# Performance work log

Measured on AMD Instinct MI355X. Metric: run time of the kernel, lower is better.

The kernel has to match this reference:

```python
import jax, jax.numpy as jnp
import numpy as np

TTT_LR = 0.01
LN_EPS = 1e-5


def setup_inputs() -> dict:
    key = jax.random.key(0)
    ks = jax.random.split(key, 4)
    B, S, D, DS = 4, 2048, 1024, 64
    sc = 1.0 / np.sqrt(D).astype(np.float32)
    return {
        "x": jax.random.normal(ks[0], (B, S, D), dtype=jnp.float32),
        "Wk": jax.random.normal(ks[1], (DS, D), dtype=jnp.float32) * sc,
        "bk": jnp.zeros((DS,), jnp.float32),
        "Wv": jax.random.normal(ks[2], (D, D), dtype=jnp.float32) * sc,
        "bv": jnp.zeros((D,), jnp.float32),
        "Wq": jax.random.normal(ks[3], (DS, D), dtype=jnp.float32) * sc,
        "bq": jnp.zeros((DS,), jnp.float32),
        "gamma": jnp.ones((D,), jnp.float32),
        "beta": jnp.zeros((D,), jnp.float32),
    }


def reference(x, Wk, bk, Wv, bv, Wq, bq, gamma, beta):
    B, S, D = x.shape
    DS = Wk.shape[0]
    # LayerNorm over last dim
    mu = jnp.mean(x, axis=-1, keepdims=True)
    var = jnp.mean((x - mu) ** 2, axis=-1, keepdims=True)
    h = (x - mu) * jax.lax.rsqrt(var + LN_EPS) * gamma + beta
    # projections: keys/queries (B,S,DS), values (B,S,D)
    keys = jnp.einsum('bsd,ed->bse', h, Wk) + bk
    values = jnp.einsum('bsd,ed->bse', h, Wv) + bv
    queries = jnp.einsum('bsd,ed->bse', h, Wq) + bq

    def step(W, qkv):
        # W: (B, D, DS) fast-weight state
        q_t, k_t, v_t = qkv  # (B,DS), (B,DS), (B,D)
        y_t = jnp.einsum('bds,bs->bd', W, q_t)      # read with query
        pred = jnp.einsum('bds,bs->bd', W, k_t)     # predict with key
        err = pred - v_t                             # (B, D)
        W = W - TTT_LR * err[:, :, None] * k_t[:, None, :]  # rank-1 grad step
        return W, y_t

    W0 = jnp.zeros((B, D, DS), x.dtype)
    # scan over time: inputs as (S, B, ...)
    qs = jnp.swapaxes(queries, 0, 1)
    ks_ = jnp.swapaxes(keys, 0, 1)
    vs = jnp.swapaxes(values, 0, 1)
    _, ys = jax.lax.scan(step, W0, (qs, ks_, vs))   # ys: (S, B, D)
    y = jnp.swapaxes(ys, 0, 1)
    return x + y
```

## Files before the change

### kernel.cpp

```cpp
#include <hip/hip_runtime.h>
#include <hip/hip_bf16.h>

#define TTT_LR 0.01f
#define LN_EPS 1e-5f

#define BB 4
#define SS 2048
#define DD 1024
#define DSZ 64
#define CHUNK 64
#define NC (SS / CHUNK)
#define NCAT 1152
#define MiB (1024ull * 1024ull)

typedef __hip_bfloat16 bf16;
typedef __bf16 bf16x8 __attribute__((ext_vector_type(8)));
typedef float f32x4 __attribute__((ext_vector_type(4)));

__device__ __forceinline__ void gload_lds16(const void* g, void* l) {
    __builtin_amdgcn_global_load_lds(
        (const __attribute__((address_space(1))) unsigned int*)g,
        (__attribute__((address_space(3))) unsigned int*)l, 16, 0, 0);
}

__global__ __launch_bounds__(256) void cvt_cat_kernel(
    const float* __restrict__ Wk, const float* __restrict__ Wq,
    const float* __restrict__ Wv, bf16* __restrict__ Wcat)
{
    const int i = blockIdx.x * 256 + threadIdx.x;
    if (i >= NCAT * DD / 4) return;
    const int idx = i * 4;
    const int row = idx >> 10, col = idx & 1023;
    const float* src = (row < 64)  ? (Wk + (size_t)row * DD)
                     : (row < 128) ? (Wq + (size_t)(row - 64) * DD)
                                   : (Wv + (size_t)(row - 128) * DD);
    float4 v = *reinterpret_cast<const float4*>(src + col);
    bf16 h4[4] = {__float2bfloat16(v.x), __float2bfloat16(v.y),
                  __float2bfloat16(v.z), __float2bfloat16(v.w)};
    *reinterpret_cast<ushort4*>(Wcat + idx) = *reinterpret_cast<ushort4*>(h4);
}

__global__ __launch_bounds__(256) void ln_kernel(
    const float* __restrict__ x, const float* __restrict__ gamma,
    const float* __restrict__ beta, bf16* __restrict__ hb)
{
    __shared__ float wsum[4], wsum2[4];
    const int row = blockIdx.x, tid = threadIdx.x;
    const int lane = tid & 63, wave = tid >> 6;

    float4 v0 = *reinterpret_cast<const float4*>(x + (size_t)row * DD + tid * 4);
    float s = v0.x + v0.y + v0.z + v0.w;
    float s2 = fmaf(v0.x, v0.x, fmaf(v0.y, v0.y, fmaf(v0.z, v0.z, v0.w * v0.w)));
    #pragma unroll
    for (int off = 32; off > 0; off >>= 1) {
        s  += __shfl_down(s, off, 64);
        s2 += __shfl_down(s2, off, 64);
    }
    if (lane == 0) { wsum[wave] = s; wsum2[wave] = s2; }
    __syncthreads();
    s  = wsum[0] + wsum[1] + wsum[2] + wsum[3];
    s2 = wsum2[0] + wsum2[1] + wsum2[2] + wsum2[3];
    const float mu = s * (1.0f / DD);
    const float rs = rsqrtf(s2 * (1.0f / DD) - mu * mu + LN_EPS);

    float4 g  = *reinterpret_cast<const float4*>(gamma + tid * 4);
    float4 be = *reinterpret_cast<const float4*>(beta + tid * 4);
    bf16 h4[4];
    h4[0] = __float2bfloat16((v0.x - mu) * rs * g.x + be.x);
    h4[1] = __float2bfloat16((v0.y - mu) * rs * g.y + be.y);
    h4[2] = __float2bfloat16((v0.z - mu) * rs * g.z + be.z);
    h4[3] = __float2bfloat16((v0.w - mu) * rs * g.w + be.w);
    *reinterpret_cast<ushort4*>(hb + (size_t)row * DD + tid * 4) =
        *reinterpret_cast<ushort4*>(h4);
}

__global__ __launch_bounds__(256) void kqv_kernel(
    const bf16* __restrict__ h, const bf16* __restrict__ Wcat,
    const float* __restrict__ bk, const float* __restrict__ bq,
    const float* __restrict__ bv,
    float* __restrict__ kbuf, float* __restrict__ qbuf, bf16* __restrict__ vbuf16)
{
    __shared__ bf16 Ash[128 * 64];
    __shared__ bf16 Bsh[128 * 64];
    const int tid = threadIdx.x, lane = tid & 63, wave = tid >> 6;
    const int m = lane & 15, quad = lane >> 4;
    const int wr = wave >> 1, wc = wave & 1;
    const int m0 = blockIdx.y * 128;
    const int n0 = blockIdx.x * 128;

    const int srow = wave * 8 + (lane >> 3);
    const int scb = lane & 7;

    f32x4 acc[4][4] = {};

    for (int k0 = 0; k0 < DD; k0 += 64) {
        __syncthreads();
        #pragma unroll
        for (int i = 0; i < 4; ++i) {
            const int row = i * 32 + srow;
            const int g16 = scb ^ (row & 7);
            gload_lds16(h    + (size_t)(m0 + row) * DD + k0 + g16 * 8,
                        (char*)Ash + (size_t)(i * 32 + wave * 8) * 128);
            gload_lds16(Wcat + (size_t)(n0 + row) * DD + k0 + g16 * 8,
                        (char*)Bsh + (size_t)(i * 32 + wave * 8) * 128);
        }
        __syncthreads();
        #pragma unroll
        for (int ks = 0; ks < 2; ++ks) {
            bf16x8 af[4], bfr[4];
            #pragma unroll
            for (int mt = 0; mt < 4; ++mt) {
                const int row = wr * 64 + mt * 16 + m;
                const int kb = (ks * 4 + quad) ^ (row & 7);
                af[mt] = *reinterpret_cast<const bf16x8*>(&Ash[row * 64 + kb * 8]);
            }
            #pragma unroll
            for (int nt = 0; nt < 4; ++nt) {
                const int row = wc * 64 + nt * 16 + m;
                const int kb = (ks * 4 + quad) ^ (row & 7);
                bfr[nt] = *reinterpret_cast<const bf16x8*>(&Bsh[row * 64 + kb * 8]);
            }
            #pragma unroll
            for (int mt = 0; mt < 4; ++mt)
                #pragma unroll
                for (int nt = 0; nt < 4; ++nt)
                    acc[mt][nt] = __builtin_amdgcn_mfma_f32_16x16x32_bf16(
                        af[mt], bfr[nt], acc[mt][nt], 0, 0, 0);
        }
    }

    #pragma unroll
    for (int nt = 0; nt < 4; ++nt) {
        const int n = n0 + wc * 64 + nt * 16 + m;
        if (n < 64) {
            const float bias = bk[n];
            #pragma unroll
            for (int mt = 0; mt < 4; ++mt) {
                const int row = m0 + wr * 64 + mt * 16 + quad * 4;
                #pragma unroll
                for (int r = 0; r < 4; ++r)
                    kbuf[(size_t)(row + r) * DSZ + n] = acc[mt][nt][r] + bias;
            }
        } else if (n < 128) {
            const float bias = bq[n - 64];
            #pragma unroll
            for (int mt = 0; mt < 4; ++mt) {
                const int row = m0 + wr * 64 + mt * 16 + quad * 4;
                #pragma unroll
                for (int r = 0; r < 4; ++r)
                    qbuf[(size_t)(row + r) * DSZ + (n - 64)] = acc[mt][nt][r] + bias;
            }
        } else {
            const float bias = bv[n - 128];
            #pragma unroll
            for (int mt = 0; mt < 4; ++mt) {
                const int row = m0 + wr * 64 + mt * 16 + quad * 4;
                #pragma unroll
                for (int r = 0; r < 4; ++r)
                    vbuf16[(size_t)(row + r) * DD + (n - 128)] =
                        __float2bfloat16(acc[mt][nt][r] + bias);
            }
        }
    }
}

__global__ __launch_bounds__(256) void prep_kernel(
    const float* __restrict__ kbuf, const float* __restrict__ qbuf,
    bf16* __restrict__ Mb16, bf16* __restrict__ AMb16,
    bf16* __restrict__ Bb16, bf16* __restrict__ Qtb16, bf16* __restrict__ Ktb16)
{
    __shared__ bf16 K16[64 * 72];
    __shared__ bf16 Kt16[64 * 72];
    __shared__ bf16 Q16[64 * 72];
    __shared__ bf16 Astl[64 * 72];
    __shared__ bf16 Minv16[64 * 72];
    __shared__ bf16 MinvT16[64 * 72];
    __shared__ bf16 BnegT[64 * 72];
    __shared__ float Gf[64 * 65];
    __shared__ float Mf[64 * 65];

    const int c = blockIdx.x, b = blockIdx.y;
    const int tid = threadIdx.x, lane = tid & 63, w = tid >> 6;
    const int m = lane & 15, quad = lane >> 4;
    const float* kp = kbuf + ((size_t)b * SS + c * 64) * DSZ;
    const float* qp = qbuf + ((size_t)b * SS + c * 64) * DSZ;
    const size_t cb = ((size_t)b * NC + c) * 4096;

    #pragma unroll
    for (int it = 0; it < 4; ++it) {
        const int f4 = tid + it * 256;
        const int t = f4 >> 4;
        const int s = (f4 & 15) * 4;
        float4 kv = *reinterpret_cast<const float4*>(kp + t * DSZ + s);
        float4 qv = *reinterpret_cast<const float4*>(qp + t * DSZ + s);
        bf16 kb4[4] = {__float2bfloat16(kv.x), __float2bfloat16(kv.y),
                       __float2bfloat16(kv.z), __float2bfloat16(kv.w)};
        bf16 qb4[4] = {__float2bfloat16(qv.x), __float2bfloat16(qv.y),
                       __float2bfloat16(qv.z), __float2bfloat16(qv.w)};
        *reinterpret_cast<ushort4*>(&K16[t * 72 + s]) = *reinterpret_cast<ushort4*>(kb4);
        *reinterpret_cast<ushort4*>(&Q16[t * 72 + s]) = *reinterpret_cast<ushort4*>(qb4);
        #pragma unroll
        for (int i = 0; i < 4; ++i) Kt16[(s + i) * 72 + t] = kb4[i];
    }
    __syncthreads();

    bf16x8 afK[2], afQ[2], bfK[4][2];
    #pragma unroll
    for (int ks = 0; ks < 2; ++ks) {
        afK[ks] = *reinterpret_cast<const bf16x8*>(&K16[(w * 16 + m) * 72 + ks * 32 + quad * 8]);
        afQ[ks] = *reinterpret_cast<const bf16x8*>(&Q16[(w * 16 + m) * 72 + ks * 32 + quad * 8]);
        #pragma unroll
        for (int nt = 0; nt < 4; ++nt)
            bfK[nt][ks] = *reinterpret_cast<const bf16x8*>(&K16[(nt * 16 + m) * 72 + ks * 32 + quad * 8]);
    }
    f32x4 gacc[4] = {}, aacc[4] = {};
    #pragma unroll
    for (int ks = 0; ks < 2; ++ks)
        #pragma unroll
        for (int nt = 0; nt < 4; ++nt) {
            gacc[nt] = __builtin_amdgcn_mfma_f32_16x16x32_bf16(afK[ks], bfK[nt][ks], gacc[nt], 0, 0, 0);
            aacc[nt] = __builtin_amdgcn_mfma_f32_16x16x32_bf16(afQ[ks], bfK[nt][ks], aacc[nt], 0, 0, 0);
        }
    #pragma unroll
    for (int nt = 0; nt < 4; ++nt)
        #pragma unroll
        for (int r = 0; r < 4; ++r) {
            const int t = w * 16 + quad * 4 + r, j = nt * 16 + m;
            Gf[t * 65 + j] = TTT_LR * gacc[nt][r];
            Astl[t * 72 + j] = __float2bfloat16(j < t ? aacc[nt][r] : 0.f);
        }
    __syncthreads();

    if (tid < 64) {
        for (int t = 0; t < 64; ++t) {
            float acc = (t == tid) ? 1.f : 0.f;
            for (int i = 0; i < t; ++i)
                acc = fmaf(-Gf[t * 65 + i], Mf[i * 65 + tid], acc);
            Mf[t * 65 + tid] = acc;
        }
    }
    __syncthreads();

    #pragma unroll
    for (int it = 0; it < 16; ++it) {
        const int e = tid + it * 256;
        const int t = e >> 6, j = e & 63;
        const bf16 vb = __float2bfloat16(TTT_LR * Mf[t * 65 + j]);
        Minv16[t * 72 + j] = vb;
        MinvT16[j * 72 + t] = vb;
        Mb16[cb + e] = vb;
        const unsigned short ku =
            *reinterpret_cast<const unsigned short*>(&Kt16[t * 72 + j]) ^ 0x8000u;
        *reinterpret_cast<unsigned short*>(&Ktb16[cb + e]) = ku;
    }
    __syncthreads();

    bf16x8 afM[2], afA[2], bfKt[4][2], bfMt[4][2];
    #pragma unroll
    for (int ks = 0; ks < 2; ++ks) {
        afM[ks] = *reinterpret_cast<const bf16x8*>(&Minv16[(w * 16 + m) * 72 + ks * 32 + quad * 8]);
        afA[ks] = *reinterpret_cast<const bf16x8*>(&Astl[(w * 16 + m) * 72 + ks * 32 + quad * 8]);
        #pragma unroll
        for (int nt = 0; nt < 4; ++nt) {
            bfKt[nt][ks] = *reinterpret_cast<const bf16x8*>(&Kt16[(nt * 16 + m) * 72 + ks * 32 + quad * 8]);
            bfMt[nt][ks] = *reinterpret_cast<const bf16x8*>(&MinvT16[(nt * 16 + m) * 72 + ks * 32 + quad * 8]);
        }
    }
    f32x4 bacc[4] = {};
    #pragma unroll
    for (int ks = 0; ks < 2; ++ks)
        #pragma unroll
        for (int nt = 0; nt < 4; ++nt)
            bacc[nt] = __builtin_amdgcn_mfma_f32_16x16x32_bf16(afM[ks], bfKt[nt][ks], bacc[nt], 0, 0, 0);
    #pragma unroll
    for (int nt = 0; nt < 4; ++nt)
        #pragma unroll
        for (int r = 0; r < 4; ++r) {
            const int t = w * 16 + quad * 4 + r, s = nt * 16 + m;
            Bb16[cb + t * 64 + s] = __float2bfloat16(bacc[nt][r]);
            BnegT[s * 72 + t] = __float2bfloat16(-bacc[nt][r]);
        }
    __syncthreads();

    f32x4 qtacc[4], amacc[4] = {};
    #pragma unroll
    for (int nt = 0; nt < 4; ++nt)
        #pragma unroll
        for (int r = 0; r < 4; ++r)
            qtacc[nt][r] = qp[(w * 16 + quad * 4 + r) * DSZ + nt * 16 + m];
    #pragma unroll
    for (int ks = 0; ks < 2; ++ks)
        #pragma unroll
        for (int nt = 0; nt < 4; ++nt) {
            const bf16x8 bfBn = *reinterpret_cast<const bf16x8*>(
                &BnegT[(nt * 16 + m) * 72 + ks * 32 + quad * 8]);
            qtacc[nt] = __builtin_amdgcn_mfma_f32_16x16x32_bf16(afA[ks], bfBn, qtacc[nt], 0, 0, 0);
            amacc[nt] = __builtin_amdgcn_mfma_f32_16x16x32_bf16(afA[ks], bfMt[nt][ks], amacc[nt], 0, 0, 0);
        }
    #pragma unroll
    for (int nt = 0; nt < 4; ++nt)
        #pragma unroll
        for (int r = 0; r < 4; ++r) {
            const int t = w * 16 + quad * 4 + r, s = nt * 16 + m;
            Qtb16[cb + t * 64 + s] = __float2bfloat16(qtacc[nt][r]);
            AMb16[cb + t * 64 + s] = __float2bfloat16(amacc[nt][r]);
        }
}

__global__ __launch_bounds__(256) void scan2_kernel(
    const bf16* __restrict__ Mb16, const bf16* __restrict__ AMb16,
    const bf16* __restrict__ Bb16, const bf16* __restrict__ Qtb16,
    const bf16* __restrict__ Ktb16, const bf16* __restrict__ v16,
    const float* __restrict__ x, float* __restrict__ out)
{
    __shared__ bf16 Zsh[16][72];
    __shared__ bf16 Psh[16][72];
    __shared__ bf16 Vsh[2][16][72];
    const int dblk = blockIdx.x, b = blockIdx.y;
    const int tid = threadIdx.x, lane = tid & 63, w = tid >> 6;
    const int m = lane & 15, quad = lane >> 4;
    const int d0 = dblk * 16;
    const int arow = w * 16 + m;
    const int trow = w * 16 + quad * 4;

    const int vj = tid >> 2;
    const int vd = (tid & 3) * 4;

    f32x4 zacc = {0.f, 0.f, 0.f, 0.f};
    for (int i = tid; i < 16 * 72; i += 256)
        (&Zsh[0][0])[i] = __float2bfloat16(0.f);

    for (int c = 0; c < NC; ++c) {
        const size_t cb = ((size_t)b * NC + c) * 4096;
        const size_t rowbase = (size_t)b * SS + (size_t)c * 64;
        const size_t gbase = (rowbase + trow) * DD + d0 + m;

        const bf16x8 aM0 = *reinterpret_cast<const bf16x8*>(Mb16 + cb + arow * 64 + quad * 8);
        const bf16x8 aM1 = *reinterpret_cast<const bf16x8*>(Mb16 + cb + arow * 64 + 32 + quad * 8);
        const bf16x8 aA0 = *reinterpret_cast<const bf16x8*>(AMb16 + cb + arow * 64 + quad * 8);
        const bf16x8 aA1 = *reinterpret_cast<const bf16x8*>(AMb16 + cb + arow * 64 + 32 + quad * 8);
        const bf16x8 aB0 = *reinterpret_cast<const bf16x8*>(Bb16 + cb + arow * 64 + quad * 8);
        const bf16x8 aB1 = *reinterpret_cast<const bf16x8*>(Bb16 + cb + arow * 64 + 32 + quad * 8);
        const bf16x8 aQ0 = *reinterpret_cast<const bf16x8*>(Qtb16 + cb + arow * 64 + quad * 8);
        const bf16x8 aQ1 = *reinterpret_cast<const bf16x8*>(Qtb16 + cb + arow * 64 + 32 + quad * 8);
        const bf16x8 aK0 = *reinterpret_cast<const bf16x8*>(Ktb16 + cb + arow * 64 + quad * 8);
        const bf16x8 aK1 = *reinterpret_cast<const bf16x8*>(Ktb16 + cb + arow * 64 + 32 + quad * 8);
        alignas(8) bf16 va[4];
        *reinterpret_cast<uint2*>(va) = *reinterpret_cast<const uint2*>(
            v16 + (rowbase + vj) * DD + d0 + vd);
        float xld[4];
        #pragma unroll
        for (int r = 0; r < 4; ++r) xld[r] = x[gbase + (size_t)r * DD];

        #pragma unroll
        for (int i = 0; i < 4; ++i) Vsh[c & 1][vd + i][vj] = va[i];

        __syncthreads();
        const bf16x8 z0 = *reinterpret_cast<const bf16x8*>(&Zsh[m][quad * 8]);
        const bf16x8 z1 = *reinterpret_cast<const bf16x8*>(&Zsh[m][32 + quad * 8]);
        const bf16x8 v0 = *reinterpret_cast<const bf16x8*>(&Vsh[c & 1][m][quad * 8]);
        const bf16x8 v1 = *reinterpret_cast<const bf16x8*>(&Vsh[c & 1][m][32 + quad * 8]);

        f32x4 uacc = {0.f, 0.f, 0.f, 0.f};
        f32x4 yi   = {0.f, 0.f, 0.f, 0.f};
        f32x4 pacc = {0.f, 0.f, 0.f, 0.f};
        f32x4 yc   = {0.f, 0.f, 0.f, 0.f};
        uacc = __builtin_amdgcn_mfma_f32_16x16x32_bf16(aM0, v0, uacc, 0, 0, 0);
        uacc = __builtin_amdgcn_mfma_f32_16x16x32_bf16(aM1, v1, uacc, 0, 0, 0);
        yi   = __builtin_amdgcn_mfma_f32_16x16x32_bf16(aA0, v0, yi, 0, 0, 0);
        yi   = __builtin_amdgcn_mfma_f32_16x16x32_bf16(aA1, v1, yi, 0, 0, 0);
        pacc = __builtin_amdgcn_mfma_f32_16x16x32_bf16(aB0, z0, pacc, 0, 0, 0);
        pacc = __builtin_amdgcn_mfma_f32_16x16x32_bf16(aB1, z1, pacc, 0, 0, 0);
        yc   = __builtin_amdgcn_mfma_f32_16x16x32_bf16(aQ0, z0, yc, 0, 0, 0);
        yc   = __builtin_amdgcn_mfma_f32_16x16x32_bf16(aQ1, z1, yc, 0, 0, 0);

        alignas(8) bf16 pb[4];
        #pragma unroll
        for (int r = 0; r < 4; ++r) {
            out[gbase + (size_t)r * DD] = xld[r] + yi[r] + yc[r];
            pb[r] = __float2bfloat16(pacc[r] - uacc[r]);
        }
        *reinterpret_cast<uint2*>(&Psh[m][trow]) = *reinterpret_cast<uint2*>(pb);

        __syncthreads();
        const bf16x8 p0 = *reinterpret_cast<const bf16x8*>(&Psh[m][quad * 8]);
        const bf16x8 p1 = *reinterpret_cast<const bf16x8*>(&Psh[m][32 + quad * 8]);
        zacc = __builtin_amdgcn_mfma_f32_16x16x32_bf16(aK0, p0, zacc, 0, 0, 0);
        zacc = __builtin_amdgcn_mfma_f32_16x16x32_bf16(aK1, p1, zacc, 0, 0, 0);

        alignas(8) bf16 zb[4];
        #pragma unroll
        for (int r = 0; r < 4; ++r) zb[r] = __float2bfloat16(zacc[r]);
        *reinterpret_cast<uint2*>(&Zsh[m][trow]) = *reinterpret_cast<uint2*>(zb);
    }
}

extern "C" void kernel_launch(void* const* d_in, const int* in_sizes, int n_in,
                              void* d_out, int out_size, void* d_ws, size_t ws_size,
                              hipStream_t stream)
{
    const float* x     = (const float*)d_in[0];
    const float* Wk    = (const float*)d_in[1];
    const float* bk    = (const float*)d_in[2];
    const float* Wv    = (const float*)d_in[3];
    const float* bv    = (const float*)d_in[4];
    const float* Wq    = (const float*)d_in[5];
    const float* bq    = (const float*)d_in[6];
    const float* gamma = (const float*)d_in[7];
    const float* beta  = (const float*)d_in[8];

    char* ws = (char*)d_ws;
    const size_t WCAT_B = (size_t)NCAT * DD * 2;
    bf16*  hb    = (bf16*)ws;
    bf16*  Bb16  = (bf16*)(ws + 0 * MiB);
    bf16*  Qtb16 = (bf16*)(ws + 1 * MiB);
    bf16*  Ktb16 = (bf16*)(ws + 2 * MiB);
    bf16*  Mb16  = (bf16*)(ws + 3 * MiB);
    bf16*  AMb16 = (bf16*)(ws + 4 * MiB);
    bf16*  Wcat  = (bf16*)(ws + 16 * MiB);
    float* kbuf  = (float*)(ws + 16 * MiB + WCAT_B);
    float* qbuf  = (float*)(ws + 18 * MiB + WCAT_B);
    bf16*  v16   = (bf16*)(ws + 20 * MiB + WCAT_B);

    cvt_cat_kernel<<<(NCAT * DD / 4 + 255) / 256, 256, 0, stream>>>(Wk, Wq, Wv, Wcat);
    ln_kernel<<<BB * SS, 256, 0, stream>>>(x, gamma, beta, hb);
    kqv_kernel<<<dim3(NCAT / 128, BB * SS / 128), 256, 0, stream>>>(
        hb, Wcat, bk, bq, bv, kbuf, qbuf, v16);
    prep_kernel<<<dim3(NC, BB), 256, 0, stream>>>(
        kbuf, qbuf, Mb16, AMb16, Bb16, Qtb16, Ktb16);
    scan2_kernel<<<dim3(DD / 16, BB), 256, 0, stream>>>(
        Mb16, AMb16, Bb16, Qtb16, Ktb16, v16, x, (float*)d_out);
}
```

Baseline: 233.4 us.

## Software-pipeline scan chunk loads and merge weight-convert into layernorm kernel

The scan kernel now prefetches the next chunk's operand fragments, V tile and x values into registers while computing the current chunk, using two register sets and an unrolled-by-two loop. This hides global load latency on the sequential chunk chain. The V staging is reworked so half the threads write packed 32-bit pairs to shared memory. The weight bf16 conversion and layernorm kernels are merged into one launch to save a launch. The prefetching raises register pressure, which may lower occupancy.

```diff
diff --git a/kernel.cpp b/kernel.cpp
--- a/kernel.cpp
+++ b/kernel.cpp
@@ -11,6 +11,7 @@
 #define CHUNK 64
 #define NC (SS / CHUNK)
 #define NCAT 1152
+#define NCVT (NCAT * DD / 4 / 256)
 #define MiB (1024ull * 1024ull)
 
 typedef __hip_bfloat16 bf16;
@@ -23,29 +24,30 @@
         (__attribute__((address_space(3))) unsigned int*)l, 16, 0, 0);
 }
 
-__global__ __launch_bounds__(256) void cvt_cat_kernel(
+__global__ __launch_bounds__(256) void pre_kernel(
     const float* __restrict__ Wk, const float* __restrict__ Wq,
-    const float* __restrict__ Wv, bf16* __restrict__ Wcat)
-{
-    const int i = blockIdx.x * 256 + threadIdx.x;
-    if (i >= NCAT * DD / 4) return;
-    const int idx = i * 4;
-    const int row = idx >> 10, col = idx & 1023;
-    const float* src = (row < 64)  ? (Wk + (size_t)row * DD)
-                     : (row < 128) ? (Wq + (size_t)(row - 64) * DD)
-                                   : (Wv + (size_t)(row - 128) * DD);
-    float4 v = *reinterpret_cast<const float4*>(src + col);
-    bf16 h4[4] = {__float2bfloat16(v.x), __float2bfloat16(v.y),
-                  __float2bfloat16(v.z), __float2bfloat16(v.w)};
-    *reinterpret_cast<ushort4*>(Wcat + idx) = *reinterpret_cast<ushort4*>(h4);
-}
-
-__global__ __launch_bounds__(256) void ln_kernel(
+    const float* __restrict__ Wv, bf16* __restrict__ Wcat,
     const float* __restrict__ x, const float* __restrict__ gamma,
     const float* __restrict__ beta, bf16* __restrict__ hb)
 {
     __shared__ float wsum[4], wsum2[4];
-    const int row = blockIdx.x, tid = threadIdx.x;
+    const int tid = threadIdx.x;
+
+    if (blockIdx.x < NCVT) {
+        const int i = blockIdx.x * 256 + tid;
+        const int idx = i * 4;
+        const int row = idx >> 10, col = idx & 1023;
+        const float* src = (row < 64)  ? (Wk + (size_t)row * DD)
+                         : (row < 128) ? (Wq + (size_t)(row - 64) * DD)
+                                       : (Wv + (size_t)(row - 128) * DD);
+        float4 v = *reinterpret_cast<const float4*>(src + col);
+        bf16 h4[4] = {__float2bfloat16(v.x), __float2bfloat16(v.y),
+                      __float2bfloat16(v.z), __float2bfloat16(v.w)};
+        *reinterpret_cast<ushort4*>(Wcat + idx) = *reinterpret_cast<ushort4*>(h4);
+        return;
+    }
+
+    const int row = blockIdx.x - NCVT;
     const int lane = tid & 63, wave = tid >> 6;
 
     float4 v0 = *reinterpret_cast<const float4*>(x + (size_t)row * DD + tid * 4);
@@ -306,6 +308,12 @@
             AMb16[cb + t * 64 + s] = __float2bfloat16(amacc[nt][r]);
         }
 }
+
+struct ChunkRegs {
+    bf16x8 M0, M1, A0, A1, B0, B1, Q0, Q1, K0, K1;
+    alignas(8) unsigned short va[4], vb[4];
+    float xld[4];
+};
 
 __global__ __launch_bounds__(256) void scan2_kernel(
     const bf16* __restrict__ Mb16, const bf16* __restrict__ AMb16,
@@ -323,61 +331,73 @@
     const int arow = w * 16 + m;
     const int trow = w * 16 + quad * 4;
 
-    const int vj = tid >> 2;
-    const int vd = (tid & 3) * 4;
+    const bool vact = tid < 128;
+    const int vj2 = (tid & 31) * 2;
+    const int vd = (tid >> 5) * 4;
 
     f32x4 zacc = {0.f, 0.f, 0.f, 0.f};
     for (int i = tid; i < 16 * 72; i += 256)
         (&Zsh[0][0])[i] = __float2bfloat16(0.f);
 
-    for (int c = 0; c < NC; ++c) {
+    auto load_chunk = [&](int c, ChunkRegs& R) {
         const size_t cb = ((size_t)b * NC + c) * 4096;
         const size_t rowbase = (size_t)b * SS + (size_t)c * 64;
+        R.M0 = *reinterpret_cast<const bf16x8*>(Mb16 + cb + arow * 64 + quad * 8);
+        R.M1 = *reinterpret_cast<const bf16x8*>(Mb16 + cb + arow * 64 + 32 + quad * 8);
+        R.A0 = *reinterpret_cast<const bf16x8*>(AMb16 + cb + arow * 64 + quad * 8);
+        R.A1 = *reinterpret_cast<const bf16x8*>(AMb16 + cb + arow * 64 + 32 + quad * 8);
+        R.B0 = *reinterpret_cast<const bf16x8*>(Bb16 + cb + arow * 64 + quad * 8);
+        R.B1 = *reinterpret_cast<const bf16x8*>(Bb16 + cb + arow * 64 + 32 + quad * 8);
+        R.Q0 = *reinterpret_cast<const bf16x8*>(Qtb16 + cb + arow * 64 + quad * 8);
+        R.Q1 = *reinterpret_cast<const bf16x8*>(Qtb16 + cb + arow * 64 + 32 + quad * 8);
+        R.K0 = *reinterpret_cast<const bf16x8*>(Ktb16 + cb + arow * 64 + quad * 8);
+        R.K1 = *reinterpret_cast<const bf16x8*>(Ktb16 + cb + arow * 64 + 32 + quad * 8);
+        if (vact) {
+            *reinterpret_cast<uint2*>(R.va) = *reinterpret_cast<const uint2*>(
+                v16 + (rowbase + vj2) * DD + d0 + vd);
+            *reinterpret_cast<uint2*>(R.vb) = *reinterpret_cast<const uint2*>(
+                v16 + (rowbase + vj2 + 1) * DD + d0 + vd);
+        }
         const size_t gbase = (rowbase + trow) * DD + d0 + m;
-
-        const bf16x8 aM0 = *reinterpret_cast<const bf16x8*>(Mb16 + cb + arow * 64 + quad * 8);
-        const bf16x8 aM1 = *reinterpret_cast<const bf16x8*>(Mb16 + cb + arow * 64 + 32 + quad * 8);
-        const bf16x8 aA0 = *reinterpret_cast<const bf16x8*>(AMb16 + cb + arow * 64 + quad * 8);
-        const bf16x8 aA1 = *reinterpret_cast<const bf16x8*>(AMb16 + cb + arow * 64 + 32 + quad * 8);
-        const bf16x8 aB0 = *reinterpret_cast<const bf16x8*>(Bb16 + cb + arow * 64 + quad * 8);
-        const bf16x8 aB1 = *reinterpret_cast<const bf16x8*>(Bb16 + cb + arow * 64 + 32 + quad * 8);
-        const bf16x8 aQ0 = *reinterpret_cast<const bf16x8*>(Qtb16 + cb + arow * 64 + quad * 8);
-        const bf16x8 aQ1 = *reinterpret_cast<const bf16x8*>(Qtb16 + cb + arow * 64 + 32 + quad * 8);
-        const bf16x8 aK0 = *reinterpret_cast<const bf16x8*>(Ktb16 + cb + arow * 64 + quad * 8);
-        const bf16x8 aK1 = *reinterpret_cast<const bf16x8*>(Ktb16 + cb + arow * 64 + 32 + quad * 8);
-        alignas(8) bf16 va[4];
-        *reinterpret_cast<uint2*>(va) = *reinterpret_cast<const uint2*>(
-            v16 + (rowbase + vj) * DD + d0 + vd);
-        float xld[4];
-        #pragma unroll
-        for (int r = 0; r < 4; ++r) xld[r] = x[gbase + (size_t)r * DD];
-
-        #pragma unroll
-        for (int i = 0; i < 4; ++i) Vsh[c & 1][vd + i][vj] = va[i];
-
-        __syncthreads();
+        #pragma unroll
+        for (int r = 0; r < 4; ++r) R.xld[r] = x[gbase + (size_t)r * DD];
+    };
+
+    auto stage_v = [&](const ChunkRegs& R, int buf) {
+        if (vact) {
+            #pragma unroll
+            for (int i = 0; i < 4; ++i) {
+                const unsigned int pack =
+                    (unsigned int)R.va[i] | ((unsigned int)R.vb[i] << 16);
+                *reinterpret_cast<unsigned int*>(&Vsh[buf][vd + i][vj2]) = pack;
+            }
+        }
+    };
+
+    auto compute = [&](const ChunkRegs& R, int c, int buf) {
+        const size_t gbase = ((size_t)b * SS + (size_t)c * 64 + trow) * DD + d0 + m;
         const bf16x8 z0 = *reinterpret_cast<const bf16x8*>(&Zsh[m][quad * 8]);
         const bf16x8 z1 = *reinterpret_cast<const bf16x8*>(&Zsh[m][32 + quad * 8]);
-        const bf16x8 v0 = *reinterpret_cast<const bf16x8*>(&Vsh[c & 1][m][quad * 8]);
-        const bf16x8 v1 = *reinterpret_cast<const bf16x8*>(&Vsh[c & 1][m][32 + quad * 8]);
+        const bf16x8 v0 = *reinterpret_cast<const bf16x8*>(&Vsh[buf][m][quad * 8]);
+        const bf16x8 v1 = *reinterpret_cast<const bf16x8*>(&Vsh[buf][m][32 + quad * 8]);
 
         f32x4 uacc = {0.f, 0.f, 0.f, 0.f};
         f32x4 yi   = {0.f, 0.f, 0.f, 0.f};
         f32x4 pacc = {0.f, 0.f, 0.f, 0.f};
         f32x4 yc   = {0.f, 0.f, 0.f, 0.f};
-        uacc = __builtin_amdgcn_mfma_f32_16x16x32_bf16(aM0, v0, uacc, 0, 0, 0);
-        uacc = __builtin_amdgcn_mfma_f32_16x16x32_bf16(aM1, v1, uacc, 0, 0, 0);
-        yi   = __builtin_amdgcn_mfma_f32_16x16x32_bf16(aA0, v0, yi, 0, 0, 0);
-        yi   = __builtin_amdgcn_mfma_f32_16x16x32_bf16(aA1, v1, yi, 0, 0, 0);
-        pacc = __builtin_amdgcn_mfma_f32_16x16x32_bf16(aB0, z0, pacc, 0, 0, 0);
-        pacc = __builtin_amdgcn_mfma_f32_16x16x32_bf16(aB1, z1, pacc, 0, 0, 0);
-        yc   = __builtin_amdgcn_mfma_f32_16x16x32_bf16(aQ0, z0, yc, 0, 0, 0);
-        yc   = __builtin_amdgcn_mfma_f32_16x16x32_bf16(aQ1, z1, yc, 0, 0, 0);
+        uacc = __builtin_amdgcn_mfma_f32_16x16x32_bf16(R.M0, v0, uacc, 0, 0, 0);
+        uacc = __builtin_amdgcn_mfma_f32_16x16x32_bf16(R.M1, v1, uacc, 0, 0, 0);
+        yi   = __builtin_amdgcn_mfma_f32_16x16x32_bf16(R.A0, v0, yi, 0, 0, 0);
+        yi   = __builtin_amdgcn_mfma_f32_16x16x32_bf16(R.A1, v1, yi, 0, 0, 0);
+        pacc = __builtin_amdgcn_mfma_f32_16x16x32_bf16(R.B0, z0, pacc, 0, 0, 0);
+        pacc = __builtin_amdgcn_mfma_f32_16x16x32_bf16(R.B1, z1, pacc, 0, 0, 0);
+        yc   = __builtin_amdgcn_mfma_f32_16x16x32_bf16(R.Q0, z0, yc, 0, 0, 0);
+        yc   = __builtin_amdgcn_mfma_f32_16x16x32_bf16(R.Q1, z1, yc, 0, 0, 0);
 
         alignas(8) bf16 pb[4];
         #pragma unroll
         for (int r = 0; r < 4; ++r) {
-            out[gbase + (size_t)r * DD] = xld[r] + yi[r] + yc[r];
+            out[gbase + (size_t)r * DD] = R.xld[r] + yi[r] + yc[r];
             pb[r] = __float2bfloat16(pacc[r] - uacc[r]);
         }
         *reinterpret_cast<uint2*>(&Psh[m][trow]) = *reinterpret_cast<uint2*>(pb);
@@ -385,13 +405,26 @@
         __syncthreads();
         const bf16x8 p0 = *reinterpret_cast<const bf16x8*>(&Psh[m][quad * 8]);
         const bf16x8 p1 = *reinterpret_cast<const bf16x8*>(&Psh[m][32 + quad * 8]);
-        zacc = __builtin_amdgcn_mfma_f32_16x16x32_bf16(aK0, p0, zacc, 0, 0, 0);
-        zacc = __builtin_amdgcn_mfma_f32_16x16x32_bf16(aK1, p1, zacc, 0, 0, 0);
+        zacc = __builtin_amdgcn_mfma_f32_16x16x32_bf16(R.K0, p0, zacc, 0, 0, 0);
+        zacc = __builtin_amdgcn_mfma_f32_16x16x32_bf16(R.K1, p1, zacc, 0, 0, 0);
 
         alignas(8) bf16 zb[4];
         #pragma unroll
         for (int r = 0; r < 4; ++r) zb[r] = __float2bfloat16(zacc[r]);
         *reinterpret_cast<uint2*>(&Zsh[m][trow]) = *reinterpret_cast<uint2*>(zb);
+    };
+
+    ChunkRegs R0, R1;
+    load_chunk(0, R0);
+    for (int c = 0; c < NC; c += 2) {
+        stage_v(R0, 0);
+        __syncthreads();
+        load_chunk(c + 1, R1);
+        compute(R0, c, 0);
+        stage_v(R1, 1);
+        __syncthreads();
+        if (c + 2 < NC) load_chunk(c + 2, R0);
+        compute(R1, c + 1, 1);
     }
 }
 
@@ -422,8 +455,8 @@
     float* qbuf  = (float*)(ws + 18 * MiB + WCAT_B);
     bf16*  v16   = (bf16*)(ws + 20 * MiB + WCAT_B);
 
-    cvt_cat_kernel<<<(NCAT * DD / 4 + 255) / 256, 256, 0, stream>>>(Wk, Wq, Wv, Wcat);
-    ln_kernel<<<BB * SS, 256, 0, stream>>>(x, gamma, beta, hb);
+    pre_kernel<<<NCVT + BB * SS, 256, 0, stream>>>(
+        Wk, Wq, Wv, Wcat, x, gamma, beta, hb);
     kqv_kernel<<<dim3(NCAT / 128, BB * SS / 128), 256, 0, stream>>>(
         hb, Wcat, bk, bq, bv, kbuf, qbuf, v16);
     prep_kernel<<<dim3(NC, BB), 256, 0, stream>>>(
```

New measurement: 229.3 us. No clear change (-1.8%).
